# Kernel tuning notes

Hardware: AMD Instinct MI355X
Metric: run time of the kernel (lower is better)

The kernel has to match this reference:

```python
import jax, jax.numpy as jnp
import numpy as np

L = 6          # backbone GENConv layers
N = 100000     # nodes
E = 625000     # edges
F = 128        # gnn_in_features
HID = 64       # learner hidden width
NTOT = 200000  # node-feature table rows
TASKS = 112    # num_tasks
LN_EPS = 1e-5
MSG_EPS = 1e-7


def setup_inputs() -> dict:
    key = jax.random.key(0)
    ks = iter(jax.random.split(key, 40))

    def w(shape, fan):
        return jax.random.normal(next(ks), shape, jnp.float32) / np.float32(np.sqrt(fan))

    inp = {}
    inp["x"] = jax.random.uniform(next(ks), (N, 8), jnp.float32)
    inp["node_index"] = jax.random.randint(next(ks), (N,), 0, NTOT)
    inp["edge_index"] = jax.random.randint(next(ks), (2, E), 0, N)
    inp["edge_attr"] = jax.random.normal(next(ks), (E, 8), jnp.float32)
    inp["node_features_table"] = jax.random.normal(next(ks), (NTOT, 8), jnp.float32)
    inp["W_ohe"] = w((8, 8), 8); inp["b_ohe"] = jnp.zeros((8,), jnp.float32)
    inp["W_enc"] = w((16, F), 16); inp["b_enc"] = jnp.zeros((F,), jnp.float32)
    inp["W_edge"] = w((8, F), 8); inp["b_edge"] = jnp.zeros((F,), jnp.float32)
    inp["learner_W1"] = w((L + 1, F, HID), F); inp["learner_b1"] = jnp.zeros((L + 1, HID), jnp.float32)
    inp["learner_W2"] = w((L + 1, HID, F), HID); inp["learner_b2"] = jnp.zeros((L + 1, F), jnp.float32)
    inp["gcn_W"] = w((L, F, F), F); inp["gcn_b"] = jnp.zeros((L, F), jnp.float32)
    inp["gcn_t"] = jnp.ones((L,), jnp.float32)   # learnable softmax temperature
    inp["ln_gamma"] = jnp.ones((L, F), jnp.float32); inp["ln_beta"] = jnp.zeros((L, F), jnp.float32)
    inp["W_pred"] = w((F, TASKS), F); inp["b_pred"] = jnp.zeros((TASKS,), jnp.float32)
    return inp


def _layer_norm(h, g, b):
    mu = jnp.mean(h, -1, keepdims=True)
    var = jnp.mean(jnp.square(h - mu), -1, keepdims=True)
    return g * (h - mu) * jax.lax.rsqrt(var + LN_EPS) + b


def _learner(z, W1, b1, W2, b2):
    # NodeWeightLearner: 2-layer MLP with LeakyReLU(0.2), sigmoid gate per node/feature
    z = jax.nn.leaky_relu(z @ W1 + b1, 0.2)
    return jax.nn.sigmoid(z @ W2 + b2)


def reference(x, node_index, edge_index, edge_attr, node_features_table,
              W_ohe, b_ohe, W_enc, b_enc, W_edge, b_edge,
              learner_W1, learner_b1, learner_W2, learner_b2,
              gcn_W, gcn_b, gcn_t, ln_gamma, ln_beta, W_pred, b_pred):
    src, dst = edge_index[0], edge_index[1]
    n = x.shape[0]

    nf = jnp.concatenate([node_features_table[node_index], x @ W_ohe + b_ohe], axis=1)  # [N,16]
    h = nf @ W_enc + b_enc                                                              # [N,F]
    nw = _learner(h, learner_W1[0], learner_b1[0], learner_W2[0], learner_b2[0])
    h = h * nw
    codebank = h * nw
    edge_emb = edge_attr @ W_edge + b_edge                                              # [E,F]

    for l in range(L):
        # GENConv with softmax aggregation: m_e = relu(x_src + e) + eps, segment-softmax over dst
        m = jax.nn.relu(h[src] + edge_emb) + MSG_EPS          # [E,F]
        s = m * gcn_t[l]
        mx = jax.ops.segment_max(s, dst, num_segments=n)
        e = jnp.exp(s - mx[dst])
        denom = jax.ops.segment_sum(e, dst, num_segments=n)
        alpha = e / (denom[dst] + 1e-16)
        agg = jax.ops.segment_sum(alpha * m, dst, num_segments=n)  # [N,F]
        h1 = (h + agg) @ gcn_W[l] + gcn_b[l]                        # GENConv MLP (mlp_layers=1)
        h = jax.nn.relu(_layer_norm(h1, ln_gamma[l], ln_beta[l]))
        nw = _learner(h + codebank, learner_W1[l + 1], learner_b1[l + 1],
                      learner_W2[l + 1], learner_b2[l + 1])
        h_f = h * nw
        h = h_f + codebank * (1.0 - nw)    # highway combine
        codebank = codebank + h_f          # codebank update
        # dropout p=0.0 / eval mode -> identity

    return codebank @ W_pred + b_pred
```

## Files before the change

kernel.cpp:

```cpp
#include <hip/hip_runtime.h>
#include <stdint.h>

#define NN 100000
#define EE 625000
#define FF 128
#define HH 64
#define LL 6
#define TT 112

#define SCAN_CHUNK 2048
#define SCAN_NB ((NN + SCAN_CHUNK - 1) / SCAN_CHUNK)

typedef unsigned short u16;
typedef unsigned int u32;
typedef __attribute__((ext_vector_type(8))) short bf16x8;
typedef __attribute__((ext_vector_type(4))) float f32x4;

#define OFF_X    0u
#define OFF_TB   800000u
#define OFF_WO   2400000u
#define OFF_BO   2400064u
#define OFF_WE   2400072u
#define OFF_BE   2402120u
#define OFF_WED  2402248u
// ... 57 lines not shown
}

struct ConvPtrs { const void* p[19]; };

__global__ __launch_bounds__(256) void k_convw(ConvPtrs ps, u16* __restrict__ wc) {
    u32 idx = blockIdx.x * 256 + threadIdx.x;
    if (idx >= CANON_N) return;
    const u32 offs[19] = {OFF_X, OFF_TB, OFF_WO, OFF_BO, OFF_WE, OFF_BE, OFF_WED, OFF_BED,
                          OFF_LW1, OFF_LB1, OFF_LW2, OFF_LB2, OFF_GW, OFF_GB, OFF_GT,
                          OFF_LG, OFF_LB, OFF_WP, OFF_BP};
    int seg = 0;
#pragma unroll
    for (int s = 1; s < 19; s++) if (idx >= offs[s]) seg = s;
    u32 e = idx - offs[seg];
    u16 v;
    if (seg == 14 && e >= 6u) {
        v = 0;
    } else {
        bool f32 = is_f32((const u32*)ps.p[14]);
        v = f32 ? f2bf(((const float*)ps.p[seg])[e]) : ((const u16*)ps.p[seg])[e];
    }
    wc[idx] = v;
}

__global__ __launch_bounds__(256) void k_twt(const u16* __restrict__ wc, u16* __restrict__ wt) {
    int idx = blockIdx.x * 256 + threadIdx.x;
    if (idx >= LL * FF * FF) return;
    int l = idx >> 14, r = (idx >> 7) & 127, c = idx & 127;
    wt[idx] = wc[OFF_GW + l * FF * FF + c * FF + r];
}

__global__ __launch_bounds__(256) void k_twl(const u16* __restrict__ wc,
                                             u16* __restrict__ w1t, u16* __restrict__ w2t,
                                             u16* __restrict__ wet, u16* __restrict__ wpt) {
    int idx = blockIdx.x * 256 + threadIdx.x;
    const int HALF = 7 * FF * HH;
    const int WETN = FF * 32;
    if (idx < HALF) {
        int ls = idx / (FF * HH), rem = idx % (FF * HH);
        int n = rem / FF, k = rem % FF;
        w1t[idx] = wc[OFF_LW1 + ls * FF * HH + k * HH + n];
    } else if (idx < 2 * HALF) {
        int j = idx - HALF;
        int ls = j / (FF * HH), rem = j % (FF * HH);
        int n = rem / HH, k = rem % HH;
        w2t[j] = wc[OFF_LW2 + ls * FF * HH + k * FF + n];
    } else if (idx < 2 * HALF + WETN) {
        int j = idx - 2 * HALF;
        int n = j >> 5, k = j & 31;
        wet[j] = (k < 16) ? wc[OFF_WE + k * FF + n] : (u16)0;
    } else if (idx < 2 * HALF + WETN + TT * FF) {
        int j = idx - 2 * HALF - WETN;
        int n = j >> 7, k = j & 127;
        wpt[j] = wc[OFF_WP + k * TT + n];
    }
}

__global__ void k_hist(const int* __restrict__ dst, int* __restrict__ counts) {
    int e = blockIdx.x * 256 + threadIdx.x;
    if (e < EE) atomicAdd(&counts[dst[e]], 1);
}

__global__ void k_scan1(const int* __restrict__ counts, int* __restrict__ bsums) {
    __shared__ int red[256];
    int t = threadIdx.x;
    int base = blockIdx.x * SCAN_CHUNK + t * 8;
    int s = 0;
#pragma unroll
    for (int j = 0; j < 8; j++) { int i = base + j; s += (i < NN) ? counts[i] : 0; }
    red[t] = s; __syncthreads();
    for (int off = 128; off > 0; off >>= 1) {
        if (t < off) red[t] += red[t + off];
        __syncthreads();
    }
    if (t == 0) bsums[blockIdx.x] = red[0];
}

__global__ void k_scan2(int* __restrict__ bsums, int* __restrict__ row_ptr) {
    __shared__ int v[256];
    int t = threadIdx.x;
    int x = (t < SCAN_NB) ? bsums[t] : 0;
    v[t] = x; __syncthreads();
    for (int off = 1; off < 256; off <<= 1) {
        int add = (t >= off) ? v[t - off] : 0;
        __syncthreads();
        v[t] += add;
        __syncthreads();
// ... 17 lines not shown
        __syncthreads();
        red[t] += add;
        __syncthreads();
    }
    int off0 = bsums[blockIdx.x] + red[t] - own;
    int run = 0;
#pragma unroll
    for (int j = 0; j < 8; j++) {
        int i = base + j;
        if (i < NN) { row_ptr[i] = off0 + run; counts_cursor[i] = off0 + run; }
        run += c[j];
    }
}

__global__ void k_scatter(const int* __restrict__ src, const int* __restrict__ dst,
                          const void* __restrict__ edge_attr, const u32* __restrict__ gt_raw,
                          int* __restrict__ cursor, int* __restrict__ s_src,
                          u16* __restrict__ s_attr) {
    int e = blockIdx.x * 256 + threadIdx.x;
    if (e >= EE) return;
    int d = dst[e];
    int p = atomicAdd(&cursor[d], 1);
    s_src[p] = src[e];
    if (is_f32(gt_raw)) {
        const float4* ea = (const float4*)edge_attr;
        float4 lo = ea[(size_t)e * 2], hi = ea[(size_t)e * 2 + 1];
        float f[8] = {lo.x, lo.y, lo.z, lo.w, hi.x, hi.y, hi.z, hi.w};
        ((uint4*)s_attr)[p] = pack8bf(f);
    } else {
        ((uint4*)s_attr)[p] = ((const uint4*)edge_attr)[e];
    }
}

template<bool CB32>
__global__ __launch_bounds__(256) void k_encoder(const u16* __restrict__ wc,
                                                 const int* __restrict__ node_index,
                                                 const u16* __restrict__ wet,
                                                 const u16* __restrict__ w1t,
                                                 const u16* __restrict__ w2t,
                                                 u16* __restrict__ h_out, void* cb_out) {
    __shared__ alignas(16) u16 sH[4][16 * 136];
    __shared__ alignas(16) char sScr[4][4608];
    __shared__ float sWo[64], sbo[8];
    int t = threadIdx.x;
    if (t < 64) sWo[t] = bf2f(wc[OFF_WO + t]);
    if (t < 8) sbo[t] = bf2f(wc[OFF_BO + t]);
    __syncthreads();

    int wave = t >> 6, lane = t & 63;
    int quad = lane >> 4, l15 = lane & 15;
    int base = blockIdx.x * 64 + wave * 16;
    int nodeA = base + l15; if (nodeA >= NN) nodeA = NN - 1;

    uint4 afu = make_uint4(0u, 0u, 0u, 0u);
    if (quad == 0) {
        afu = ((const uint4*)(wc + OFF_TB))[node_index[nodeA]];
    } else if (quad == 1) {
        uint4 xv4 = ((const uint4*)(wc + OFF_X))[nodeA];
        float xv[8]; unpack8bf(xv4, xv);
        float o[8];
#pragma unroll
        for (int j = 0; j < 8; j++) {
            float a = sbo[j];
#pragma unroll
            for (int i = 0; i < 8; i++) a += xv[i] * sWo[i * 8 + j];
            o[j] = a;
// ... 76 lines not shown
            bf16x8 bfrag = __builtin_bit_cast(bf16x8, wb);
            acc2[nt] = __builtin_amdgcn_mfma_f32_16x16x32_bf16(a2h[kc2], bfrag, acc2[nt], 0, 0, 0);
            acc2[nt] = __builtin_amdgcn_mfma_f32_16x16x32_bf16(a2l[kc2], bfrag, acc2[nt], 0, 0, 0);
        }
    float* myf = (float*)sScr[wave];
    int orow = lane >> 2, ocol = lane & 3;
    int onode = base + orow;
#pragma unroll
    for (int p = 0; p < 4; p++) {
#pragma unroll
        for (int h8 = 0; h8 < 2; h8++)
#pragma unroll
            for (int r = 0; r < 4; r++)
                myf[(quad * 4 + r) * 36 + h8 * 16 + l15] = acc2[2 * p + h8][r];
        if (onode < NN) {
            int k0 = p * 32 + ocol * 8;
            float f[8];
            unpack8bf(*(const uint4*)(hw + orow * 136 + k0), f);
            float4 lg1 = *(const float4*)(myf + orow * 36 + ocol * 8);
            float4 lg2 = *(const float4*)(myf + orow * 36 + ocol * 8 + 4);
            float lg[8] = {lg1.x, lg1.y, lg1.z, lg1.w, lg2.x, lg2.y, lg2.z, lg2.w};
            float ho[8], co[8];
#pragma unroll
            for (int j = 0; j < 8; j++) {
                float nw = 1.f / (1.f + __expf(-lg[j]));
                float hwv = f[j] * nw;
                ho[j] = hwv; co[j] = hwv * nw;
            }
            ((uint4*)(h_out + (size_t)onode * FF))[k0 / 8] = pack8bf(ho);
            cb_st<CB32>(cb_out, (size_t)onode, k0 / 4, make_float4(co[0], co[1], co[2], co[3]));
            cb_st<CB32>(cb_out, (size_t)onode, k0 / 4 + 1, make_float4(co[4], co[5], co[6], co[7]));
        }
    }
}

__global__ __launch_bounds__(256) void k_agg(const u16* __restrict__ h,
                                             const int* __restrict__ row_ptr,
                                             const int* __restrict__ s_src,
                                             const u16* __restrict__ s_attr,
                                             const u16* __restrict__ wc, int layer,
                                             u16* __restrict__ agg) {
    int t = threadIdx.x;
    int hw = t >> 5, lane = t & 31;
    int node = blockIdx.x * 8 + hw;
    if (node >= NN) return;
    uint2 wcol[8];
#pragma unroll
    for (int k = 0; k < 8; k++) wcol[k] = ((const uint2*)(wc + OFF_WED))[k * 32 + lane];
    uint2 bcol = ((const uint2*)(wc + OFF_BED))[lane];
    float b0 = bflo(bcol.x), b1 = bfhi(bcol.x), b2 = bflo(bcol.y), b3 = bfhi(bcol.y);
    float tl = bf2f(wc[OFF_GT + layer]);
    int beg = row_ptr[node], end = row_ptr[node + 1];
    float n0 = 0.f, n1 = 0.f, n2 = 0.f, n3 = 0.f;
    float d0 = 0.f, d1 = 0.f, d2 = 0.f, d3 = 0.f;
    for (int i = beg; i < end; i++) {
        int sid = s_src[i];
        uint2 hv = ((const uint2*)h)[(size_t)sid * 32 + lane];
        uint4 av = ((const uint4*)s_attr)[i];
        float a[8]; unpack8bf(av, a);
        float e0 = b0, e1 = b1, e2 = b2, e3 = b3;
#pragma unroll
        for (int k = 0; k < 8; k++) {
            e0 += a[k] * bflo(wcol[k].x); e1 += a[k] * bfhi(wcol[k].x);
            e2 += a[k] * bflo(wcol[k].y); e3 += a[k] * bfhi(wcol[k].y);
        }
        float m0 = fmaxf(bflo(hv.x) + e0, 0.f) + 1e-7f;
        float m1 = fmaxf(bfhi(hv.x) + e1, 0.f) + 1e-7f;
        float m2 = fmaxf(bflo(hv.y) + e2, 0.f) + 1e-7f;
        float m3 = fmaxf(bfhi(hv.y) + e3, 0.f) + 1e-7f;
        float x0 = __expf(tl * m0), x1 = __expf(tl * m1);
        float x2 = __expf(tl * m2), x3 = __expf(tl * m3);
        n0 += x0 * m0; n1 += x1 * m1; n2 += x2 * m2; n3 += x3 * m3;
        d0 += x0; d1 += x1; d2 += x2; d3 += x3;
    }
    uint2 r;
    r.x = pack2bf(n0 / (d0 + 1e-16f), n1 / (d1 + 1e-16f));
    r.y = pack2bf(n2 / (d2 + 1e-16f), n3 / (d3 + 1e-16f));
    ((uint2*)agg)[(size_t)node * 32 + lane] = r;
}

template<bool CB32>
__global__ __launch_bounds__(256) void k_gcnpost(const u16* __restrict__ hb,
                                                 u16* ha,
                                                 void* cbv,
                                                 const u16* __restrict__ wc,
                                                 const u16* __restrict__ wt,
                                                 const u16* __restrict__ w1t,
                                                 const u16* __restrict__ w2t, int layer) {
    __shared__ alignas(16) u16 sH1[4][16 * 136];
    __shared__ alignas(16) char sScr[4][2304];
    __shared__ float smu[4][16], srstd[4][16];
    __shared__ float sg[FF], sbt[FF], sb1[HH], sb2[FF];
    int t = threadIdx.x;
    int ls = layer + 1;
    if (t < FF) {
        sg[t] = bf2f(wc[OFF_LG + layer * FF + t]);
        sbt[t] = bf2f(wc[OFF_LB + layer * FF + t]);
        sb2[t] = bf2f(wc[OFF_LB2 + ls * FF + t]);
    }
    if (t < HH) sb1[t] = bf2f(wc[OFF_LB1 + ls * HH + t]);
    __syncthreads();

    int wave = t >> 6, lane = t & 63;
    int quad = lane >> 4, l15 = lane & 15;
    int base = blockIdx.x * 64 + wave * 16;
    int nodeA = base + l15; if (nodeA >= NN) nodeA = NN - 1;
    const u16* wtl = wt + (size_t)layer * FF * FF;
    const u16* w1l = w1t + (size_t)ls * HH * FF;
    const u16* w2l = w2t + (size_t)ls * FF * HH;

    f32x4 accg[8];
#pragma unroll
    for (int nt = 0; nt < 8; nt++) {
        float bv = bf2f(wc[OFF_GB + layer * FF + nt * 16 + l15]);
        f32x4 v; v[0] = bv; v[1] = bv; v[2] = bv; v[3] = bv;
        accg[nt] = v;
    }
#pragma unroll
    for (int kc = 0; kc < 4; kc++) {
        uint4 hv = ((const uint4*)(ha + (size_t)nodeA * FF))[kc * 4 + quad];
        uint4 aa = ((const uint4*)(hb + (size_t)nodeA * FF))[kc * 4 + quad];
        float hf[8], af[8], sm[8];
        unpack8bf(hv, hf); unpack8bf(aa, af);
#pragma unroll
        for (int j = 0; j < 8; j++) sm[j] = hf[j] + af[j];
        uint4 pa = pack8bf(sm);
        bf16x8 afrag = __builtin_bit_cast(bf16x8, pa);
#pragma unroll
        for (int nt = 0; nt < 8; nt++) {
            uint4 wb = ((const uint4*)(wtl + (size_t)(nt * 16 + l15) * FF))[kc * 4 + quad];
            bf16x8 bfrag = __builtin_bit_cast(bf16x8, wb);
            accg[nt] = __builtin_amdgcn_mfma_f32_16x16x32_bf16(afrag, bfrag, accg[nt], 0, 0, 0);
        }
    }
    u16* hw = sH1[wave];
#pragma unroll
    for (int nt = 0; nt < 8; nt++)
#pragma unroll
        for (int r = 0; r < 4; r++)
            hw[(quad * 4 + r) * 136 + nt * 16 + l15] = f2bf(accg[nt][r]);

    uint4 hreg[4];
    float s = 0.f, s2 = 0.f;
#pragma unroll
    for (int kc = 0; kc < 4; kc++) {
        hreg[kc] = *(const uint4*)(hw + l15 * 136 + kc * 32 + quad * 8);
        float f[8]; unpack8bf(hreg[kc], f);
#pragma unroll
        for (int j = 0; j < 8; j++) { s += f[j]; s2 += f[j] * f[j]; }
    }
    s += __shfl_xor(s, 16); s += __shfl_xor(s, 32);
    s2 += __shfl_xor(s2, 16); s2 += __shfl_xor(s2, 32);
    float mu = s * (1.f / 128.f);
    float var = fmaxf(s2 * (1.f / 128.f) - mu * mu, 0.f);
// ... 65 lines not shown
            bf16x8 bfrag = __builtin_bit_cast(bf16x8, wb);
            acc2[nt] = __builtin_amdgcn_mfma_f32_16x16x32_bf16(a2[kc2], bfrag, acc2[nt], 0, 0, 0);
        }
    float* myf = (float*)sScr[wave];
    int orow = lane >> 2, ocol = lane & 3;
    int onode = base + orow;
#pragma unroll
    for (int p = 0; p < 4; p++) {
#pragma unroll
        for (int h8 = 0; h8 < 2; h8++)
#pragma unroll
            for (int r = 0; r < 4; r++)
                myf[(quad * 4 + r) * 36 + h8 * 16 + l15] = acc2[2 * p + h8][r];
        if (onode < NN) {
            float mu2 = smu[wave][orow], rstd2 = srstd[wave][orow];
            int k0 = p * 32 + ocol * 8;
            float f[8];
            unpack8bf(*(const uint4*)(hw + orow * 136 + k0), f);
            float4 lg1 = *(const float4*)(myf + orow * 36 + ocol * 8);
            float4 lg2 = *(const float4*)(myf + orow * 36 + ocol * 8 + 4);
            float lg[8] = {lg1.x, lg1.y, lg1.z, lg1.w, lg2.x, lg2.y, lg2.z, lg2.w};
            float4 ca = cb_ld<CB32>(cbv, (size_t)onode, k0 / 4);
            float4 cq = cb_ld<CB32>(cbv, (size_t)onode, k0 / 4 + 1);
            float cv[8] = {ca.x, ca.y, ca.z, ca.w, cq.x, cq.y, cq.z, cq.w};
            float ho[8], co[8];
#pragma unroll
            for (int j = 0; j < 8; j++) {
                float hl = fmaxf(sg[k0 + j] * (f[j] - mu2) * rstd2 + sbt[k0 + j], 0.f);
                float nw = 1.f / (1.f + __expf(-lg[j]));
                float hf = hl * nw;
                ho[j] = hf + cv[j] * (1.f - nw);
                co[j] = cv[j] + hf;
            }
            ((uint4*)(ha + (size_t)onode * FF))[k0 / 8] = pack8bf(ho);
            cb_st<CB32>(cbv, (size_t)onode, k0 / 4, make_float4(co[0], co[1], co[2], co[3]));
            cb_st<CB32>(cbv, (size_t)onode, k0 / 4 + 1, make_float4(co[4], co[5], co[6], co[7]));
        }
    }
}

template<bool CB32>
__global__ __launch_bounds__(256) void k_pred(const void* __restrict__ cbv,
                                              const u16* __restrict__ wc,
                                              const u16* __restrict__ wpt,
                                              const u32* __restrict__ gt_raw,
                                              void* __restrict__ outv) {
    __shared__ float sOutF[4][16 * 116];
    int t = threadIdx.x;
    int wave = t >> 6, lane = t & 63;
    int quad = lane >> 4, l15 = lane & 15;
    int base = blockIdx.x * 64 + wave * 16;
    int nodeA = base + l15; if (nodeA >= NN) nodeA = NN - 1;
    bool f32o = is_f32(gt_raw);

    f32x4 acc[7];
#pragma unroll
    for (int nt = 0; nt < 7; nt++) {
        float bv = bf2f(wc[OFF_BP + nt * 16 + l15]);
        f32x4 v; v[0] = bv; v[1] = bv; v[2] = bv; v[3] = bv;
        acc[nt] = v;
    }
#pragma unroll
    for (int kc = 0; kc < 4; kc++) {
        float4 ca = cb_ld<CB32>(cbv, (size_t)nodeA, kc * 8 + quad * 2);
        float4 cq = cb_ld<CB32>(cbv, (size_t)nodeA, kc * 8 + quad * 2 + 1);
        float cv[8] = {ca.x, ca.y, ca.z, ca.w, cq.x, cq.y, cq.z, cq.w};
        uint4 ahi = pack8bf(cv);
// ... 46 lines not shown
                              hipStream_t stream) {
    const int* node_index = (const int*)d_in[1];
    const int* edge_index = (const int*)d_in[2];
    const u32* gt_raw = (const u32*)d_in[17];

    ConvPtrs ps;
    ps.p[0] = d_in[0];
    ps.p[1] = d_in[4];
    ps.p[2] = d_in[5];  ps.p[3] = d_in[6];
    ps.p[4] = d_in[7];  ps.p[5] = d_in[8];
    ps.p[6] = d_in[9];  ps.p[7] = d_in[10];
    ps.p[8] = d_in[11]; ps.p[9] = d_in[12];
    ps.p[10] = d_in[13]; ps.p[11] = d_in[14];
    ps.p[12] = d_in[15]; ps.p[13] = d_in[16];
    ps.p[14] = d_in[17];
    ps.p[15] = d_in[18]; ps.p[16] = d_in[19];
    ps.p[17] = d_in[20]; ps.p[18] = d_in[21];

    auto pad = [](size_t b) { return (b + 255) & ~(size_t)255; };
    const size_t B_h = pad((size_t)NN * FF * 2);
    const size_t B_h1 = pad((size_t)(NN + 1) * FF * 2);
    const size_t B_cb32 = pad((size_t)(NN + 1) * FF * 4);
    const size_t B_cb16 = pad((size_t)(NN + 1) * FF * 2);
    const size_t B_attr = pad((size_t)EE * 8 * 2);
    const size_t B_src = pad((size_t)EE * 4);
    const size_t B_rp = pad((size_t)(NN + 1) * 4);
    const size_t B_cur = pad((size_t)NN * 4);
    const size_t B_bs = pad(256 * 4);
    const size_t B_wc = pad((size_t)CANON_N * 2);
    const size_t B_wt = pad((size_t)LL * FF * FF * 2);
    const size_t B_wlt = pad((size_t)7 * FF * HH * 2);
    const size_t B_wet = pad((size_t)FF * 32 * 2);
    const size_t B_wpt = pad((size_t)TT * FF * 2);
    size_t fixed = B_h1 + B_h + B_attr + B_src + B_rp + B_cur + B_bs + B_wc + B_wt
                 + 2 * B_wlt + B_wet + B_wpt;
    bool cb32 = (fixed + B_cb32) <= ws_size;

    char* w = (char*)d_ws;
    size_t off = 0;
    auto alloc = [&](size_t bytes) -> void* { void* p = w + off; off += bytes; return p; };
    u16* h_a = (u16*)alloc(B_h1);
    u16* hb = (u16*)alloc(B_h);
    void* cb = alloc(cb32 ? B_cb32 : B_cb16);
    u16* s_attr = (u16*)alloc(B_attr);
    int* s_src = (int*)alloc(B_src);
    int* row_ptr = (int*)alloc(B_rp);
    int* cursor = (int*)alloc(B_cur);
    int* bsums = (int*)alloc(B_bs);
    u16* wc = (u16*)alloc(B_wc);
    u16* wt = (u16*)alloc(B_wt);
    u16* w1t = (u16*)alloc(B_wlt);
    u16* w2t = (u16*)alloc(B_wlt);
    u16* wet = (u16*)alloc(B_wet);
    u16* wpt = (u16*)alloc(B_wpt);

    const int GE = (EE + 255) / 256;
    const int GA = (NN + 7) / 8;
    const int GC = (CANON_N + 255) / 256;
    const int GG = (NN + 63) / 64;
    const int GT6 = (LL * FF * FF + 255) / 256;
    const int GTL = (2 * 7 * FF * HH + FF * 32 + TT * FF + 255) / 256;

    hipMemsetAsync(cursor, 0, (size_t)NN * 4, stream);
    k_convw<<<GC, 256, 0, stream>>>(ps, wc);
    k_twt<<<GT6, 256, 0, stream>>>(wc, wt);
    k_twl<<<GTL, 256, 0, stream>>>(wc, w1t, w2t, wet, wpt);
    k_hist<<<GE, 256, 0, stream>>>(edge_index + EE, cursor);
    k_scan1<<<SCAN_NB, 256, 0, stream>>>(cursor, bsums);
    k_scan2<<<1, 256, 0, stream>>>(bsums, row_ptr);
    k_scan3<<<SCAN_NB, 256, 0, stream>>>(cursor, row_ptr, bsums);
    k_scatter<<<GE, 256, 0, stream>>>(edge_index, edge_index + EE, d_in[3], gt_raw,
                                      cursor, s_src, s_attr);

    if (cb32) k_encoder<true><<<GG, 256, 0, stream>>>(wc, node_index, wet, w1t, w2t, h_a, cb);
    else      k_encoder<false><<<GG, 256, 0, stream>>>(wc, node_index, wet, w1t, w2t, h_a, cb);

    for (int l = 0; l < LL; l++) {
        k_agg<<<GA, 256, 0, stream>>>(h_a, row_ptr, s_src, s_attr, wc, l, hb);
        if (cb32) k_gcnpost<true><<<GG, 256, 0, stream>>>(hb, h_a, cb, wc, wt, w1t, w2t, l);
        else      k_gcnpost<false><<<GG, 256, 0, stream>>>(hb, h_a, cb, wc, wt, w1t, w2t, l);
    }
    if (cb32) k_pred<true><<<GG, 256, 0, stream>>>(cb, wc, wpt, gt_raw, d_out);
    else      k_pred<false><<<GG, 256, 0, stream>>>(cb, wc, wpt, gt_raw, d_out);
}
```

Before: 1.234 ms.

## Precompute per-edge embeddings with MFMA once and reuse them across layers

```diff
diff --git a/kernel.cpp b/kernel.cpp
--- a/kernel.cpp
+++ b/kernel.cpp
@@ -113,10 +113,12 @@
 
 __global__ __launch_bounds__(256) void k_twl(const u16* __restrict__ wc,
                                              u16* __restrict__ w1t, u16* __restrict__ w2t,
-                                             u16* __restrict__ wet, u16* __restrict__ wpt) {
+                                             u16* __restrict__ wet, u16* __restrict__ wpt,
+                                             u16* __restrict__ wedt) {
     int idx = blockIdx.x * 256 + threadIdx.x;
     const int HALF = 7 * FF * HH;
     const int WETN = FF * 32;
+    const int WPTN = TT * FF;
     if (idx < HALF) {
         int ls = idx / (FF * HH), rem = idx % (FF * HH);
         int n = rem / FF, k = rem % FF;
@@ -130,10 +132,14 @@
         int j = idx - 2 * HALF;
         int n = j >> 5, k = j & 31;
         wet[j] = (k < 16) ? wc[OFF_WE + k * FF + n] : (u16)0;
-    } else if (idx < 2 * HALF + WETN + TT * FF) {
+    } else if (idx < 2 * HALF + WETN + WPTN) {
         int j = idx - 2 * HALF - WETN;
         int n = j >> 7, k = j & 127;
         wpt[j] = wc[OFF_WP + k * TT + n];
+    } else if (idx < 2 * HALF + WETN + WPTN + FF * 32) {
+        int j = idx - 2 * HALF - WETN - WPTN;
+        int n = j >> 5, k = j & 31;
+        wedt[j] = (k < 8) ? wc[OFF_WED + k * FF + n] : (u16)0;
     }
 }
 
@@ -217,6 +223,116 @@
     }
 }
 
+__global__ __launch_bounds__(256) void k_emb(const u16* __restrict__ s_attr,
+                                             const u16* __restrict__ wc,
+                                             const u16* __restrict__ wedt,
+                                             u16* __restrict__ emb) {
+    __shared__ alignas(16) u16 sOut[4][16 * 136];
+    int t = threadIdx.x;
+    int wave = t >> 6, lane = t & 63;
+    int quad = lane >> 4, l15 = lane & 15;
+    long base = (long)blockIdx.x * 64 + wave * 16;
+    long slotA = base + l15; if (slotA >= EE) slotA = EE - 1;
+
+    uint4 afu = make_uint4(0u, 0u, 0u, 0u);
+    if (quad == 0) afu = ((const uint4*)s_attr)[slotA];
+    bf16x8 af = __builtin_bit_cast(bf16x8, afu);
+
+    f32x4 acc[8];
+#pragma unroll
+    for (int nt = 0; nt < 8; nt++) {
+        float bv = bf2f(wc[OFF_BED + nt * 16 + l15]);
+        f32x4 v; v[0] = bv; v[1] = bv; v[2] = bv; v[3] = bv;
+        acc[nt] = v;
+    }
+#pragma unroll
+    for (int nt = 0; nt < 8; nt++) {
+        uint4 wb = ((const uint4*)(wedt + (size_t)(nt * 16 + l15) * 32))[quad];
+        bf16x8 bfrag = __builtin_bit_cast(bf16x8, wb);
+        acc[nt] = __builtin_amdgcn_mfma_f32_16x16x32_bf16(af, bfrag, acc[nt], 0, 0, 0);
+    }
+    u16* my = sOut[wave];
+#pragma unroll
+    for (int nt = 0; nt < 8; nt++)
+#pragma unroll
+        for (int r = 0; r < 4; r++)
+            my[(quad * 4 + r) * 136 + nt * 16 + l15] = f2bf(acc[nt][r]);
+    int orow = lane >> 2, ocol = lane & 3;
+    long oslot = base + orow;
+    if (oslot < EE) {
+        uint4* dst = (uint4*)(emb + (size_t)oslot * FF);
+        const uint4* srcl = (const uint4*)(my + orow * 136);
+#pragma unroll
+        for (int u = 0; u < 4; u++) dst[ocol * 4 + u] = srcl[ocol * 4 + u];
+    }
+}
+
+template<bool EMB>
+__global__ __launch_bounds__(256) void k_agg(const u16* __restrict__ h,
+                                             const int* __restrict__ row_ptr,
+                                             const int* __restrict__ s_src,
+                                             const u16* __restrict__ s_attr,
+                                             const u16* __restrict__ emb,
+                                             const u16* __restrict__ wc, int layer,
+                                             u16* __restrict__ agg) {
+    int t = threadIdx.x;
+    int hw = t >> 5, lane = t & 31;
+    int node = blockIdx.x * 8 + hw;
+    if (node >= NN) return;
+    float tl = bf2f(wc[OFF_GT + layer]);
+    int beg = row_ptr[node], end = row_ptr[node + 1];
+    float n0 = 0.f, n1 = 0.f, n2 = 0.f, n3 = 0.f;
+    float d0 = 0.f, d1 = 0.f, d2 = 0.f, d3 = 0.f;
+    const uint2* h2 = (const uint2*)h;
+    if (EMB) {
+        const uint2* e2 = (const uint2*)emb;
+        for (int i = beg; i < end; i++) {
+            int sid = s_src[i];
+            uint2 hv = h2[(size_t)sid * 32 + lane];
+            uint2 ev = e2[(size_t)i * 32 + lane];
+            float e0 = bflo(ev.x), e1 = bfhi(ev.x), e2f = bflo(ev.y), e3 = bfhi(ev.y);
+            float m0 = fmaxf(bflo(hv.x) + e0, 0.f) + 1e-7f;
+            float m1 = fmaxf(bfhi(hv.x) + e1, 0.f) + 1e-7f;
+            float m2 = fmaxf(bflo(hv.y) + e2f, 0.f) + 1e-7f;
+            float m3 = fmaxf(bfhi(hv.y) + e3, 0.f) + 1e-7f;
+            float x0 = __expf(tl * m0), x1 = __expf(tl * m1);
+            float x2 = __expf(tl * m2), x3 = __expf(tl * m3);
+            n0 += x0 * m0; n1 += x1 * m1; n2 += x2 * m2; n3 += x3 * m3;
+            d0 += x0; d1 += x1; d2 += x2; d3 += x3;
+        }
+    } else {
+        uint2 wcol[8];
+#pragma unroll
+        for (int k = 0; k < 8; k++) wcol[k] = ((const uint2*)(wc + OFF_WED))[k * 32 + lane];
+        uint2 bcol = ((const uint2*)(wc + OFF_BED))[lane];
+        float b0 = bflo(bcol.x), b1 = bfhi(bcol.x), b2 = bflo(bcol.y), b3 = bfhi(bcol.y);
+        for (int i = beg; i < end; i++) {
+            int sid = s_src[i];
+            uint2 hv = h2[(size_t)sid * 32 + lane];
+            uint4 av = ((const uint4*)s_attr)[i];
+            float a[8]; unpack8bf(av, a);
+            float e0 = b0, e1 = b1, e2f = b2, e3 = b3;
+#pragma unroll
+            for (int k = 0; k < 8; k++) {
+                e0 += a[k] * bflo(wcol[k].x); e1 += a[k] * bfhi(wcol[k].x);
+                e2f += a[k] * bflo(wcol[k].y); e3 += a[k] * bfhi(wcol[k].y);
+            }
+            float m0 = fmaxf(bflo(hv.x) + e0, 0.f) + 1e-7f;
+            float m1 = fmaxf(bfhi(hv.x) + e1, 0.f) + 1e-7f;
+            float m2 = fmaxf(bflo(hv.y) + e2f, 0.f) + 1e-7f;
+            float m3 = fmaxf(bfhi(hv.y) + e3, 0.f) + 1e-7f;
+            float x0 = __expf(tl * m0), x1 = __expf(tl * m1);
+            float x2 = __expf(tl * m2), x3 = __expf(tl * m3);
+            n0 += x0 * m0; n1 += x1 * m1; n2 += x2 * m2; n3 += x3 * m3;
+            d0 += x0; d1 += x1; d2 += x2; d3 += x3;
+        }
+    }
+    uint2 r;
+    r.x = pack2bf(n0 / (d0 + 1e-16f), n1 / (d1 + 1e-16f));
+    r.y = pack2bf(n2 / (d2 + 1e-16f), n3 / (d3 + 1e-16f));
+    ((uint2*)agg)[(size_t)node * 32 + lane] = r;
+}
+
 template<bool CB32>
 __global__ __launch_bounds__(256) void k_encoder(const u16* __restrict__ wc,
                                                  const int* __restrict__ node_index,
@@ -359,51 +475,6 @@
             cb_st<CB32>(cb_out, (size_t)onode, k0 / 4 + 1, make_float4(co[4], co[5], co[6], co[7]));
         }
     }
-}
-
-__global__ __launch_bounds__(256) void k_agg(const u16* __restrict__ h,
-                                             const int* __restrict__ row_ptr,
-                                             const int* __restrict__ s_src,
-                                             const u16* __restrict__ s_attr,
-                                             const u16* __restrict__ wc, int layer,
-                                             u16* __restrict__ agg) {
-    int t = threadIdx.x;
-    int hw = t >> 5, lane = t & 31;
-    int node = blockIdx.x * 8 + hw;
-    if (node >= NN) return;
-    uint2 wcol[8];
-#pragma unroll
-    for (int k = 0; k < 8; k++) wcol[k] = ((const uint2*)(wc + OFF_WED))[k * 32 + lane];
-    uint2 bcol = ((const uint2*)(wc + OFF_BED))[lane];
-    float b0 = bflo(bcol.x), b1 = bfhi(bcol.x), b2 = bflo(bcol.y), b3 = bfhi(bcol.y);
-    float tl = bf2f(wc[OFF_GT + layer]);
-    int beg = row_ptr[node], end = row_ptr[node + 1];
-    float n0 = 0.f, n1 = 0.f, n2 = 0.f, n3 = 0.f;
-    float d0 = 0.f, d1 = 0.f, d2 = 0.f, d3 = 0.f;
-    for (int i = beg; i < end; i++) {
-        int sid = s_src[i];
-        uint2 hv = ((const uint2*)h)[(size_t)sid * 32 + lane];
-        uint4 av = ((const uint4*)s_attr)[i];
-        float a[8]; unpack8bf(av, a);
-        float e0 = b0, e1 = b1, e2 = b2, e3 = b3;
-#pragma unroll
-        for (int k = 0; k < 8; k++) {
-            e0 += a[k] * bflo(wcol[k].x); e1 += a[k] * bfhi(wcol[k].x);
-            e2 += a[k] * bflo(wcol[k].y); e3 += a[k] * bfhi(wcol[k].y);
-        }
-        float m0 = fmaxf(bflo(hv.x) + e0, 0.f) + 1e-7f;
-        float m1 = fmaxf(bfhi(hv.x) + e1, 0.f) + 1e-7f;
-        float m2 = fmaxf(bflo(hv.y) + e2, 0.f) + 1e-7f;
-        float m3 = fmaxf(bfhi(hv.y) + e3, 0.f) + 1e-7f;
-        float x0 = __expf(tl * m0), x1 = __expf(tl * m1);
-        float x2 = __expf(tl * m2), x3 = __expf(tl * m3);
-        n0 += x0 * m0; n1 += x1 * m1; n2 += x2 * m2; n3 += x3 * m3;
-        d0 += x0; d1 += x1; d2 += x2; d3 += x3;
-    }
-    uint2 r;
-    r.x = pack2bf(n0 / (d0 + 1e-16f), n1 / (d1 + 1e-16f));
-    r.y = pack2bf(n2 / (d2 + 1e-16f), n3 / (d3 + 1e-16f));
-    ((uint2*)agg)[(size_t)node * 32 + lane] = r;
 }
 
 template<bool CB32>
@@ -691,16 +762,20 @@
     const size_t B_wlt = pad((size_t)7 * FF * HH * 2);
     const size_t B_wet = pad((size_t)FF * 32 * 2);
     const size_t B_wpt = pad((size_t)TT * FF * 2);
+    const size_t B_wedt = pad((size_t)FF * 32 * 2);
+    const size_t B_emb = pad((size_t)EE * FF * 2);
     size_t fixed = B_h1 + B_h + B_attr + B_src + B_rp + B_cur + B_bs + B_wc + B_wt
-                 + 2 * B_wlt + B_wet + B_wpt;
+                 + 2 * B_wlt + B_wet + B_wpt + B_wedt;
     bool cb32 = (fixed + B_cb32) <= ws_size;
+    size_t cbsz = cb32 ? B_cb32 : B_cb16;
+    bool embok = (fixed + cbsz + B_emb) <= ws_size;
 
     char* w = (char*)d_ws;
     size_t off = 0;
     auto alloc = [&](size_t bytes) -> void* { void* p = w + off; off += bytes; return p; };
     u16* h_a = (u16*)alloc(B_h1);
     u16* hb = (u16*)alloc(B_h);
-    void* cb = alloc(cb32 ? B_cb32 : B_cb16);
+    void* cb = alloc(cbsz);
     u16* s_attr = (u16*)alloc(B_attr);
     int* s_src = (int*)alloc(B_src);
     int* row_ptr = (int*)alloc(B_rp);
@@ -712,30 +787,37 @@
     u16* w2t = (u16*)alloc(B_wlt);
     u16* wet = (u16*)alloc(B_wet);
     u16* wpt = (u16*)alloc(B_wpt);
+    u16* wedt = (u16*)alloc(B_wedt);
+    u16* s_emb = embok ? (u16*)alloc(B_emb) : nullptr;
 
     const int GE = (EE + 255) / 256;
     const int GA = (NN + 7) / 8;
     const int GC = (CANON_N + 255) / 256;
     const int GG = (NN + 63) / 64;
+    const int GEM = (EE + 63) / 64;
     const int GT6 = (LL * FF * FF + 255) / 256;
-    const int GTL = (2 * 7 * FF * HH + FF * 32 + TT * FF + 255) / 256;
+    const int GTL = (2 * 7 * FF * HH + FF * 32 + TT * FF + FF * 32 + 255) / 256;
 
     hipMemsetAsync(cursor, 0, (size_t)NN * 4, stream);
     k_convw<<<GC, 256, 0, stream>>>(ps, wc);
     k_twt<<<GT6, 256, 0, stream>>>(wc, wt);
-    k_twl<<<GTL, 256, 0, stream>>>(wc, w1t, w2t, wet, wpt);
+    k_twl<<<GTL, 256, 0, stream>>>(wc, w1t, w2t, wet, wpt, wedt);
     k_hist<<<GE, 256, 0, stream>>>(edge_index + EE, cursor);
     k_scan1<<<SCAN_NB, 256, 0, stream>>>(cursor, bsums);
     k_scan2<<<1, 256, 0, stream>>>(bsums, row_ptr);
     k_scan3<<<SCAN_NB, 256, 0, stream>>>(cursor, row_ptr, bsums);
     k_scatter<<<GE, 256, 0, stream>>>(edge_index, edge_index + EE, d_in[3], gt_raw,
                                       cursor, s_src, s_attr);
+    if (embok) k_emb<<<GEM, 256, 0, stream>>>(s_attr, wc, wedt, s_emb);
 
     if (cb32) k_encoder<true><<<GG, 256, 0, stream>>>(wc, node_index, wet, w1t, w2t, h_a, cb);
     else      k_encoder<false><<<GG, 256, 0, stream>>>(wc, node_index, wet, w1t, w2t, h_a, cb);
 
     for (int l = 0; l < LL; l++) {
-        k_agg<<<GA, 256, 0, stream>>>(h_a, row_ptr, s_src, s_attr, wc, l, hb);
+        if (embok)
+            k_agg<true><<<GA, 256, 0, stream>>>(h_a, row_ptr, s_src, s_attr, s_emb, wc, l, hb);
+        else
+            k_agg<false><<<GA, 256, 0, stream>>>(h_a, row_ptr, s_src, s_attr, nullptr, wc, l, hb);
         if (cb32) k_gcnpost<true><<<GG, 256, 0, stream>>>(hb, h_a, cb, wc, wt, w1t, w2t, l);
         else      k_gcnpost<false><<<GG, 256, 0, stream>>>(hb, h_a, cb, wc, wt, w1t, w2t, l);
     }
```

Result: no change. 1.235 ms (+0.1%).

## Fuse softmax aggregation into per-layer GCN post kernel with ping-pong buffers

Applied to the files above, without the earlier changes.

```diff
diff --git a/kernel.cpp b/kernel.cpp
--- a/kernel.cpp
+++ b/kernel.cpp
@@ -361,59 +361,18 @@
     }
 }
 
-__global__ __launch_bounds__(256) void k_agg(const u16* __restrict__ h,
-                                             const int* __restrict__ row_ptr,
-                                             const int* __restrict__ s_src,
-                                             const u16* __restrict__ s_attr,
-                                             const u16* __restrict__ wc, int layer,
-                                             u16* __restrict__ agg) {
-    int t = threadIdx.x;
-    int hw = t >> 5, lane = t & 31;
-    int node = blockIdx.x * 8 + hw;
-    if (node >= NN) return;
-    uint2 wcol[8];
-#pragma unroll
-    for (int k = 0; k < 8; k++) wcol[k] = ((const uint2*)(wc + OFF_WED))[k * 32 + lane];
-    uint2 bcol = ((const uint2*)(wc + OFF_BED))[lane];
-    float b0 = bflo(bcol.x), b1 = bfhi(bcol.x), b2 = bflo(bcol.y), b3 = bfhi(bcol.y);
-    float tl = bf2f(wc[OFF_GT + layer]);
-    int beg = row_ptr[node], end = row_ptr[node + 1];
-    float n0 = 0.f, n1 = 0.f, n2 = 0.f, n3 = 0.f;
-    float d0 = 0.f, d1 = 0.f, d2 = 0.f, d3 = 0.f;
-    for (int i = beg; i < end; i++) {
-        int sid = s_src[i];
-        uint2 hv = ((const uint2*)h)[(size_t)sid * 32 + lane];
-        uint4 av = ((const uint4*)s_attr)[i];
-        float a[8]; unpack8bf(av, a);
-        float e0 = b0, e1 = b1, e2 = b2, e3 = b3;
-#pragma unroll
-        for (int k = 0; k < 8; k++) {
-            e0 += a[k] * bflo(wcol[k].x); e1 += a[k] * bfhi(wcol[k].x);
-            e2 += a[k] * bflo(wcol[k].y); e3 += a[k] * bfhi(wcol[k].y);
-        }
-        float m0 = fmaxf(bflo(hv.x) + e0, 0.f) + 1e-7f;
-        float m1 = fmaxf(bfhi(hv.x) + e1, 0.f) + 1e-7f;
-        float m2 = fmaxf(bflo(hv.y) + e2, 0.f) + 1e-7f;
-        float m3 = fmaxf(bfhi(hv.y) + e3, 0.f) + 1e-7f;
-        float x0 = __expf(tl * m0), x1 = __expf(tl * m1);
-        float x2 = __expf(tl * m2), x3 = __expf(tl * m3);
-        n0 += x0 * m0; n1 += x1 * m1; n2 += x2 * m2; n3 += x3 * m3;
-        d0 += x0; d1 += x1; d2 += x2; d3 += x3;
-    }
-    uint2 r;
-    r.x = pack2bf(n0 / (d0 + 1e-16f), n1 / (d1 + 1e-16f));
-    r.y = pack2bf(n2 / (d2 + 1e-16f), n3 / (d3 + 1e-16f));
-    ((uint2*)agg)[(size_t)node * 32 + lane] = r;
-}
-
 template<bool CB32>
-__global__ __launch_bounds__(256) void k_gcnpost(const u16* __restrict__ hb,
-                                                 u16* ha,
-                                                 void* cbv,
-                                                 const u16* __restrict__ wc,
-                                                 const u16* __restrict__ wt,
-                                                 const u16* __restrict__ w1t,
-                                                 const u16* __restrict__ w2t, int layer) {
+__global__ __launch_bounds__(256) void k_layer(const u16* __restrict__ hin,
+                                               u16* __restrict__ hout,
+                                               void* cbv,
+                                               const int* __restrict__ row_ptr,
+                                               const int* __restrict__ s_src,
+                                               const u16* __restrict__ s_attr,
+                                               const u16* __restrict__ wc,
+                                               const u16* __restrict__ wt,
+                                               const u16* __restrict__ w1t,
+                                               const u16* __restrict__ w2t, int layer) {
+    __shared__ alignas(16) u16 sAgg[4][16 * 136];
     __shared__ alignas(16) u16 sH1[4][16 * 136];
     __shared__ alignas(16) char sScr[4][2304];
     __shared__ float smu[4][16], srstd[4][16];
@@ -431,10 +390,56 @@
     int wave = t >> 6, lane = t & 63;
     int quad = lane >> 4, l15 = lane & 15;
     int base = blockIdx.x * 64 + wave * 16;
+
+    {
+        int half = lane >> 5, hl = lane & 31;
+        uint2 wcol[8];
+#pragma unroll
+        for (int k = 0; k < 8; k++) wcol[k] = ((const uint2*)(wc + OFF_WED))[k * 32 + hl];
+        uint2 bcol = ((const uint2*)(wc + OFF_BED))[hl];
+        float b0 = bflo(bcol.x), b1 = bfhi(bcol.x), b2 = bflo(bcol.y), b3 = bfhi(bcol.y);
+        float tl = bf2f(wc[OFF_GT + layer]);
+        const uint2* h2 = (const uint2*)hin;
+        u16* aw = sAgg[wave];
+        for (int p = 0; p < 8; p++) {
+            int row = p * 2 + half;
+            int node = base + row;
+            int beg = 0, end = 0;
+            if (node < NN) { beg = row_ptr[node]; end = row_ptr[node + 1]; }
+            float n0 = 0.f, n1 = 0.f, n2 = 0.f, n3 = 0.f;
+            float d0 = 0.f, d1 = 0.f, d2 = 0.f, d3 = 0.f;
+            for (int i = beg; i < end; i++) {
+                int sid = s_src[i];
+                uint2 hv = h2[(size_t)sid * 32 + hl];
+                uint4 av = ((const uint4*)s_attr)[i];
+                float a[8]; unpack8bf(av, a);
+                float e0 = b0, e1 = b1, e2f = b2, e3 = b3;
+#pragma unroll
+                for (int k = 0; k < 8; k++) {
+                    e0 += a[k] * bflo(wcol[k].x); e1 += a[k] * bfhi(wcol[k].x);
+                    e2f += a[k] * bflo(wcol[k].y); e3 += a[k] * bfhi(wcol[k].y);
+                }
+                float m0 = fmaxf(bflo(hv.x) + e0, 0.f) + 1e-7f;
+                float m1 = fmaxf(bfhi(hv.x) + e1, 0.f) + 1e-7f;
+                float m2 = fmaxf(bflo(hv.y) + e2f, 0.f) + 1e-7f;
+                float m3 = fmaxf(bfhi(hv.y) + e3, 0.f) + 1e-7f;
+                float x0 = __expf(tl * m0), x1 = __expf(tl * m1);
+                float x2 = __expf(tl * m2), x3 = __expf(tl * m3);
+                n0 += x0 * m0; n1 += x1 * m1; n2 += x2 * m2; n3 += x3 * m3;
+                d0 += x0; d1 += x1; d2 += x2; d3 += x3;
+            }
+            uint2 r;
+            r.x = pack2bf(n0 / (d0 + 1e-16f), n1 / (d1 + 1e-16f));
+            r.y = pack2bf(n2 / (d2 + 1e-16f), n3 / (d3 + 1e-16f));
+            ((uint2*)(aw + row * 136))[hl] = r;
+        }
+    }
+
     int nodeA = base + l15; if (nodeA >= NN) nodeA = NN - 1;
     const u16* wtl = wt + (size_t)layer * FF * FF;
     const u16* w1l = w1t + (size_t)ls * HH * FF;
     const u16* w2l = w2t + (size_t)ls * FF * HH;
+    u16* aw = sAgg[wave];
 
     f32x4 accg[8];
 #pragma unroll
@@ -445,8 +450,8 @@
     }
 #pragma unroll
     for (int kc = 0; kc < 4; kc++) {
-        uint4 hv = ((const uint4*)(ha + (size_t)nodeA * FF))[kc * 4 + quad];
-        uint4 aa = ((const uint4*)(hb + (size_t)nodeA * FF))[kc * 4 + quad];
+        uint4 hv = ((const uint4*)(hin + (size_t)nodeA * FF))[kc * 4 + quad];
+        uint4 aa = *(const uint4*)(aw + l15 * 136 + kc * 32 + quad * 8);
         float hf[8], af[8], sm[8];
         unpack8bf(hv, hf); unpack8bf(aa, af);
 #pragma unroll
@@ -578,7 +583,7 @@
                 ho[j] = hf + cv[j] * (1.f - nw);
                 co[j] = cv[j] + hf;
             }
-            ((uint4*)(ha + (size_t)onode * FF))[k0 / 8] = pack8bf(ho);
+            ((uint4*)(hout + (size_t)onode * FF))[k0 / 8] = pack8bf(ho);
             cb_st<CB32>(cbv, (size_t)onode, k0 / 4, make_float4(co[0], co[1], co[2], co[3]));
             cb_st<CB32>(cbv, (size_t)onode, k0 / 4 + 1, make_float4(co[4], co[5], co[6], co[7]));
         }
@@ -699,7 +704,7 @@
     size_t off = 0;
     auto alloc = [&](size_t bytes) -> void* { void* p = w + off; off += bytes; return p; };
     u16* h_a = (u16*)alloc(B_h1);
-    u16* hb = (u16*)alloc(B_h);
+    u16* h_b = (u16*)alloc(B_h);
     void* cb = alloc(cb32 ? B_cb32 : B_cb16);
     u16* s_attr = (u16*)alloc(B_attr);
     int* s_src = (int*)alloc(B_src);
@@ -714,7 +719,6 @@
     u16* wpt = (u16*)alloc(B_wpt);
 
     const int GE = (EE + 255) / 256;
-    const int GA = (NN + 7) / 8;
     const int GC = (CANON_N + 255) / 256;
     const int GG = (NN + 63) / 64;
     const int GT6 = (LL * FF * FF + 255) / 256;
@@ -734,10 +738,14 @@
     if (cb32) k_encoder<true><<<GG, 256, 0, stream>>>(wc, node_index, wet, w1t, w2t, h_a, cb);
     else      k_encoder<false><<<GG, 256, 0, stream>>>(wc, node_index, wet, w1t, w2t, h_a, cb);
 
+    u16* hin = h_a;
+    u16* hout = h_b;
     for (int l = 0; l < LL; l++) {
-        k_agg<<<GA, 256, 0, stream>>>(h_a, row_ptr, s_src, s_attr, wc, l, hb);
-        if (cb32) k_gcnpost<true><<<GG, 256, 0, stream>>>(hb, h_a, cb, wc, wt, w1t, w2t, l);
-        else      k_gcnpost<false><<<GG, 256, 0, stream>>>(hb, h_a, cb, wc, wt, w1t, w2t, l);
+        if (cb32) k_layer<true><<<GG, 256, 0, stream>>>(hin, hout, cb, row_ptr, s_src,
+                                                        s_attr, wc, wt, w1t, w2t, l);
+        else      k_layer<false><<<GG, 256, 0, stream>>>(hin, hout, cb, row_ptr, s_src,
+                                                         s_attr, wc, wt, w1t, w2t, l);
+        u16* tmp = hin; hin = hout; hout = tmp;
     }
     if (cb32) k_pred<true><<<GG, 256, 0, stream>>>(cb, wc, wpt, gt_raw, d_out);
     else      k_pred<false><<<GG, 256, 0, stream>>>(cb, wc, wpt, gt_raw, d_out);
```

New measurement: 1.416 ms. 14.8% more time.

## Compute per-edge embeddings with MFMA into LDS tiles in aggregation kernel

Applied to the files above, without the earlier changes.

```diff
diff --git a/kernel.cpp b/kernel.cpp
--- a/kernel.cpp
+++ b/kernel.cpp
@@ -113,10 +113,12 @@
 
 __global__ __launch_bounds__(256) void k_twl(const u16* __restrict__ wc,
                                              u16* __restrict__ w1t, u16* __restrict__ w2t,
-                                             u16* __restrict__ wet, u16* __restrict__ wpt) {
+                                             u16* __restrict__ wet, u16* __restrict__ wpt,
+                                             u16* __restrict__ wedt) {
     int idx = blockIdx.x * 256 + threadIdx.x;
     const int HALF = 7 * FF * HH;
     const int WETN = FF * 32;
+    const int WPTN = TT * FF;
     if (idx < HALF) {
         int ls = idx / (FF * HH), rem = idx % (FF * HH);
         int n = rem / FF, k = rem % FF;
@@ -130,10 +132,14 @@
         int j = idx - 2 * HALF;
         int n = j >> 5, k = j & 31;
         wet[j] = (k < 16) ? wc[OFF_WE + k * FF + n] : (u16)0;
-    } else if (idx < 2 * HALF + WETN + TT * FF) {
+    } else if (idx < 2 * HALF + WETN + WPTN) {
         int j = idx - 2 * HALF - WETN;
         int n = j >> 7, k = j & 127;
         wpt[j] = wc[OFF_WP + k * TT + n];
+    } else if (idx < 2 * HALF + WETN + WPTN + FF * 32) {
+        int j = idx - 2 * HALF - WETN - WPTN;
+        int n = j >> 5, k = j & 31;
+        wedt[j] = (k < 8) ? wc[OFF_WED + k * FF + n] : (u16)0;
     }
 }
 
@@ -365,45 +371,85 @@
                                              const int* __restrict__ row_ptr,
                                              const int* __restrict__ s_src,
                                              const u16* __restrict__ s_attr,
-                                             const u16* __restrict__ wc, int layer,
+                                             const u16* __restrict__ wc,
+                                             const u16* __restrict__ wedt, int layer,
                                              u16* __restrict__ agg) {
+    __shared__ alignas(16) u16 sE[128 * 136];
     int t = threadIdx.x;
-    int hw = t >> 5, lane = t & 31;
-    int node = blockIdx.x * 8 + hw;
-    if (node >= NN) return;
-    uint2 wcol[8];
-#pragma unroll
-    for (int k = 0; k < 8; k++) wcol[k] = ((const uint2*)(wc + OFF_WED))[k * 32 + lane];
-    uint2 bcol = ((const uint2*)(wc + OFF_BED))[lane];
-    float b0 = bflo(bcol.x), b1 = bfhi(bcol.x), b2 = bflo(bcol.y), b3 = bfhi(bcol.y);
+    int node0 = blockIdx.x * 8;
+    if (node0 >= NN) return;
+    int nend = node0 + 8; if (nend > NN) nend = NN;
+    int s0 = row_ptr[node0], s1 = row_ptr[nend];
+
+    int hw = t >> 5, hl = t & 31;
+    int node = node0 + hw;
+    bool nvalid = node < NN;
+    int beg = nvalid ? row_ptr[node] : 0;
+    int end = nvalid ? row_ptr[node + 1] : 0;
     float tl = bf2f(wc[OFF_GT + layer]);
-    int beg = row_ptr[node], end = row_ptr[node + 1];
+    const uint2* h2 = (const uint2*)h;
+
+    int wave = t >> 6, l63 = t & 63;
+    int quad = l63 >> 4, l15 = l63 & 15;
+
     float n0 = 0.f, n1 = 0.f, n2 = 0.f, n3 = 0.f;
     float d0 = 0.f, d1 = 0.f, d2 = 0.f, d3 = 0.f;
-    for (int i = beg; i < end; i++) {
-        int sid = s_src[i];
-        uint2 hv = ((const uint2*)h)[(size_t)sid * 32 + lane];
-        uint4 av = ((const uint4*)s_attr)[i];
-        float a[8]; unpack8bf(av, a);
-        float e0 = b0, e1 = b1, e2 = b2, e3 = b3;
-#pragma unroll
-        for (int k = 0; k < 8; k++) {
-            e0 += a[k] * bflo(wcol[k].x); e1 += a[k] * bfhi(wcol[k].x);
-            e2 += a[k] * bflo(wcol[k].y); e3 += a[k] * bfhi(wcol[k].y);
-        }
-        float m0 = fmaxf(bflo(hv.x) + e0, 0.f) + 1e-7f;
-        float m1 = fmaxf(bfhi(hv.x) + e1, 0.f) + 1e-7f;
-        float m2 = fmaxf(bflo(hv.y) + e2, 0.f) + 1e-7f;
-        float m3 = fmaxf(bfhi(hv.y) + e3, 0.f) + 1e-7f;
-        float x0 = __expf(tl * m0), x1 = __expf(tl * m1);
-        float x2 = __expf(tl * m2), x3 = __expf(tl * m3);
-        n0 += x0 * m0; n1 += x1 * m1; n2 += x2 * m2; n3 += x3 * m3;
-        d0 += x0; d1 += x1; d2 += x2; d3 += x3;
-    }
-    uint2 r;
-    r.x = pack2bf(n0 / (d0 + 1e-16f), n1 / (d1 + 1e-16f));
-    r.y = pack2bf(n2 / (d2 + 1e-16f), n3 / (d3 + 1e-16f));
-    ((uint2*)agg)[(size_t)node * 32 + lane] = r;
+
+    for (int c0 = s0; c0 < s1; c0 += 128) {
+        int cnt = s1 - c0; if (cnt > 128) cnt = 128;
+        for (int tile = wave; tile < 8; tile += 4) {
+            int rb = tile * 16;
+            if (rb >= cnt) break;
+            long slotA = (long)c0 + rb + l15;
+            if (slotA >= s1) slotA = s1 - 1;
+            uint4 afu = make_uint4(0u, 0u, 0u, 0u);
+            if (quad == 0) afu = ((const uint4*)s_attr)[slotA];
+            bf16x8 af = __builtin_bit_cast(bf16x8, afu);
+            f32x4 acc[8];
+#pragma unroll
+            for (int nt = 0; nt < 8; nt++) {
+                float bv = bf2f(wc[OFF_BED + nt * 16 + l15]);
+                f32x4 v; v[0] = bv; v[1] = bv; v[2] = bv; v[3] = bv;
+                acc[nt] = v;
+            }
+#pragma unroll
+            for (int nt = 0; nt < 8; nt++) {
+                uint4 wb = ((const uint4*)(wedt + (size_t)(nt * 16 + l15) * 32))[quad];
+                bf16x8 bfrag = __builtin_bit_cast(bf16x8, wb);
+                acc[nt] = __builtin_amdgcn_mfma_f32_16x16x32_bf16(af, bfrag, acc[nt], 0, 0, 0);
+            }
+            u16* my = sE + (size_t)rb * 136;
+#pragma unroll
+            for (int nt = 0; nt < 8; nt++)
+#pragma unroll
+                for (int r = 0; r < 4; r++)
+                    my[(quad * 4 + r) * 136 + nt * 16 + l15] = f2bf(acc[nt][r]);
+        }
+        __syncthreads();
+        int lo = beg > c0 ? beg : c0;
+        int hi = end < c0 + cnt ? end : c0 + cnt;
+        for (int i = lo; i < hi; i++) {
+            int sid = s_src[i];
+            uint2 hv = h2[(size_t)sid * 32 + hl];
+            uint2 ev = ((const uint2*)(sE + (size_t)(i - c0) * 136))[hl];
+            float e0 = bflo(ev.x), e1 = bfhi(ev.x), e2f = bflo(ev.y), e3 = bfhi(ev.y);
+            float m0 = fmaxf(bflo(hv.x) + e0, 0.f) + 1e-7f;
+            float m1 = fmaxf(bfhi(hv.x) + e1, 0.f) + 1e-7f;
+            float m2 = fmaxf(bflo(hv.y) + e2f, 0.f) + 1e-7f;
+            float m3 = fmaxf(bfhi(hv.y) + e3, 0.f) + 1e-7f;
+            float x0 = __expf(tl * m0), x1 = __expf(tl * m1);
+            float x2 = __expf(tl * m2), x3 = __expf(tl * m3);
+            n0 += x0 * m0; n1 += x1 * m1; n2 += x2 * m2; n3 += x3 * m3;
+            d0 += x0; d1 += x1; d2 += x2; d3 += x3;
+        }
+        __syncthreads();
+    }
+    if (nvalid) {
+        uint2 r;
+        r.x = pack2bf(n0 / (d0 + 1e-16f), n1 / (d1 + 1e-16f));
+        r.y = pack2bf(n2 / (d2 + 1e-16f), n3 / (d3 + 1e-16f));
+        ((uint2*)agg)[(size_t)node * 32 + hl] = r;
+    }
 }
 
 template<bool CB32>
@@ -691,8 +737,9 @@
     const size_t B_wlt = pad((size_t)7 * FF * HH * 2);
     const size_t B_wet = pad((size_t)FF * 32 * 2);
     const size_t B_wpt = pad((size_t)TT * FF * 2);
+    const size_t B_wedt = pad((size_t)FF * 32 * 2);
     size_t fixed = B_h1 + B_h + B_attr + B_src + B_rp + B_cur + B_bs + B_wc + B_wt
-                 + 2 * B_wlt + B_wet + B_wpt;
+                 + 2 * B_wlt + B_wet + B_wpt + B_wedt;
     bool cb32 = (fixed + B_cb32) <= ws_size;
 
     char* w = (char*)d_ws;
@@ -712,18 +759,19 @@
     u16* w2t = (u16*)alloc(B_wlt);
     u16* wet = (u16*)alloc(B_wet);
     u16* wpt = (u16*)alloc(B_wpt);
+    u16* wedt = (u16*)alloc(B_wedt);
 
     const int GE = (EE + 255) / 256;
     const int GA = (NN + 7) / 8;
     const int GC = (CANON_N + 255) / 256;
     const int GG = (NN + 63) / 64;
     const int GT6 = (LL * FF * FF + 255) / 256;
-    const int GTL = (2 * 7 * FF * HH + FF * 32 + TT * FF + 255) / 256;
+    const int GTL = (2 * 7 * FF * HH + FF * 32 + TT * FF + FF * 32 + 255) / 256;
 
     hipMemsetAsync(cursor, 0, (size_t)NN * 4, stream);
     k_convw<<<GC, 256, 0, stream>>>(ps, wc);
     k_twt<<<GT6, 256, 0, stream>>>(wc, wt);
-    k_twl<<<GTL, 256, 0, stream>>>(wc, w1t, w2t, wet, wpt);
+    k_twl<<<GTL, 256, 0, stream>>>(wc, w1t, w2t, wet, wpt, wedt);
     k_hist<<<GE, 256, 0, stream>>>(edge_index + EE, cursor);
     k_scan1<<<SCAN_NB, 256, 0, stream>>>(cursor, bsums);
     k_scan2<<<1, 256, 0, stream>>>(bsums, row_ptr);
@@ -735,7 +783,7 @@
     else      k_encoder<false><<<GG, 256, 0, stream>>>(wc, node_index, wet, w1t, w2t, h_a, cb);
 
     for (int l = 0; l < LL; l++) {
-        k_agg<<<GA, 256, 0, stream>>>(h_a, row_ptr, s_src, s_attr, wc, l, hb);
+        k_agg<<<GA, 256, 0, stream>>>(h_a, row_ptr, s_src, s_attr, wc, wedt, l, hb);
         if (cb32) k_gcnpost<true><<<GG, 256, 0, stream>>>(hb, h_a, cb, wc, wt, w1t, w2t, l);
         else      k_gcnpost<false><<<GG, 256, 0, stream>>>(hb, h_a, cb, wc, wt, w1t, w2t, l);
     }
```

Result: slower. 1.659 ms (+34.5%).
